# Kernel tuning notes

Measured on AMD Instinct MI355X. Metric: run time of the kernel, lower is better.

## Reference

```python
import jax, jax.numpy as jnp
import numpy as np

B, N, D, H, DH = 1, 192, 128, 4, 32
INNER = H * DH  # == D


def _ln(x, g, b):
    mu = x.mean(-1, keepdims=True)
    var = ((x - mu) ** 2).mean(-1, keepdims=True)
    return (x - mu) * jax.lax.rsqrt(var + 1e-5) * g + b


def _axial(x, row, lng, lnb, wq, wkv, wo, bo, wg, bg, wb):
    # x: (B, N, N, D). row=True: attend along axis 2 (rows as batch);
    # row=False: attend along axis 1 (columns as batch).
    scale = DH ** -0.5
    # edge bias from RAW x (edges are not layer-normed in the torch code)
    bias = jnp.einsum('bijd,dh->bhij', x, wb)            # (B, H, N, N)
    xn = _ln(x, lng, lnb)
    xa = xn if row else jnp.swapaxes(xn, 1, 2)           # (B, R, S, D)
    q = (xa @ wq).reshape(B, N, N, H, DH) * scale
    kv = (xa @ wkv).reshape(B, N, N, 2, H, DH)           # chunk(2): k then v
    k, v = kv[..., 0, :, :], kv[..., 1, :, :]
    # scores: (B, R, H, q, k); same bias matrix broadcast over every row/col R
    dots = jnp.einsum('brqhe,brkhe->brhqk', q, k) + bias[:, None]
    attn = jax.nn.softmax(dots, axis=-1)
    o = jnp.einsum('brhqk,brkhe->brqhe', attn, v).reshape(B, N, N, INNER)
    gates = jax.nn.sigmoid(xa @ wg + bg)                 # sigmoid gating on pre-attn x
    out = (o * gates) @ wo + bo
    return out if row else jnp.swapaxes(out, 1, 2)


def setup_inputs() -> dict:
    key = jax.random.key(0)
    ks = iter(jax.random.split(key, 32))

    def w(shape, s=0.02):
        return jax.random.normal(next(ks), shape, dtype=jnp.float32) * s

    inp = {"x": jax.random.normal(next(ks), (B, N, N, D), dtype=jnp.float32)}
    for sfx in ("o", "i"):  # outgoing (row) / ingoing (col) triangle attention
        inp[f"lng_{sfx}"] = jnp.ones((D,), jnp.float32)
        inp[f"lnb_{sfx}"] = jnp.zeros((D,), jnp.float32)
        inp[f"wq_{sfx}"] = w((D, INNER))
        inp[f"wkv_{sfx}"] = w((D, 2 * INNER))
        inp[f"wo_{sfx}"] = w((INNER, D))
        inp[f"bo_{sfx}"] = jnp.zeros((D,), jnp.float32)
        inp[f"wg_{sfx}"] = w((D, INNER))
        inp[f"bg_{sfx}"] = jnp.ones((INNER,), jnp.float32)  # gating bias init = 1
        inp[f"wb_{sfx}"] = w((D, H))
    inp["lng_f"] = jnp.ones((D,), jnp.float32)
    inp["lnb_f"] = jnp.zeros((D,), jnp.float32)
    inp["w1"] = w((D, 8 * D))      # dim -> dim*mult*2, mult=4
    inp["b1"] = jnp.zeros((8 * D,), jnp.float32)
    inp["w2"] = w((4 * D, D))
    inp["b2"] = jnp.zeros((D,), jnp.float32)
    return inp


def reference(x, lng_o, lnb_o, wq_o, wkv_o, wo_o, bo_o, wg_o, bg_o, wb_o,
              lng_i, lnb_i, wq_i, wkv_i, wo_i, bo_i, wg_i, bg_i, wb_i,
              lng_f, lnb_f, w1, b1, w2, b2):
    x = _axial(x, True, lng_o, lnb_o, wq_o, wkv_o, wo_o, bo_o, wg_o, bg_o, wb_o) + x
    x = _axial(x, False, lng_i, lnb_i, wq_i, wkv_i, wo_i, bo_i, wg_i, bg_i, wb_i) + x
    xn = _ln(x, lng_f, lnb_f)
    h = xn @ w1 + b1
    a, g = jnp.split(h, 2, axis=-1)   # GEGLU: x * gelu(gates), exact gelu
    ff = (a * jax.nn.gelu(g, approximate=False)) @ w2 + b2
    return x + ff
```

## Files before the change

kernel.cpp:

```cpp
#include <hip/hip_runtime.h>
#include <hip/hip_bf16.h>
#include <math.h>

constexpr int NSEQ = 192;
constexpr int DIM  = 128;
constexpr int NH   = 4;
constexpr int DHEAD = 32;
constexpr int MROWS = NSEQ * NSEQ;

typedef __hip_bfloat16 bf16;
typedef __attribute__((ext_vector_type(8))) short bf16x8;
typedef __attribute__((ext_vector_type(4))) float f32x4;
typedef unsigned int u32;

__device__ __forceinline__ void gload16(const void* g, void* l) {
    __builtin_amdgcn_global_load_lds(
        (const __attribute__((address_space(1))) u32*)g,
        (__attribute__((address_space(3))) u32*)l, 16, 0, 0);
}

__device__ __forceinline__ short f2bs(float f) {
    __hip_bfloat16 h = __float2bfloat16(f);
    return *(short*)&h;
}
__device__ __forceinline__ float bs2f(unsigned short s) {
    return __uint_as_float(((u32)s) << 16);
}

__global__ __launch_bounds__(256)
void prep_kernel(const float* __restrict__ wq_o, const float* __restrict__ wkv_o,
                 const float* __restrict__ wg_o,
                 const float* __restrict__ wq_i, const float* __restrict__ wkv_i,
                 const float* __restrict__ wg_i,
                 const float* __restrict__ wo_o, const float* __restrict__ wo_i,
                 const float* __restrict__ w1, const float* __restrict__ b1,
                 const float* __restrict__ w2,
                 bf16* __restrict__ WQKVG_O, bf16* __restrict__ WQKVG_I,
                 bf16* __restrict__ WOT_O, bf16* __restrict__ WOT_I,
                 bf16* __restrict__ W1PT, bf16* __restrict__ W2T,
                 float* __restrict__ B1P,
                 const float* __restrict__ x, const float* __restrict__ lng,
                 const float* __restrict__ lnb, const float* __restrict__ wb,
                 bf16* __restrict__ xa, bf16* __restrict__ bias,
                 bf16* __restrict__ xb)
{
    if (blockIdx.x < 1412) {
        int idx = blockIdx.x * 256 + threadIdx.x;
        const float scale = 0.17677669529663689f;
        if (idx < 131072) {
            int s = idx >> 16, i = idx & 65535;
            int r = i >> 7, d = i & 127;
            const float* wq  = s ? wq_i  : wq_o;
            const float* wkv = s ? wkv_i : wkv_o;
            const float* wg  = s ? wg_i  : wg_o;
            float v;
            if (r < 128)      v = wq[d * 128 + r] * scale;
            else if (r < 384) v = wkv[d * 256 + (r - 128)];
            else              v = wg[d * 128 + (r - 384)];
            (s ? WQKVG_I : WQKVG_O)[i] = __float2bfloat16(v);
        } else if (idx < 163840) {
            int i = idx - 131072; int s = i >> 14; i &= 16383;
            int r = i >> 7, d = i & 127;
            (s ? WOT_I : WOT_O)[i] = __float2bfloat16((s ? wo_i : wo_o)[d * 128 + r]);
        } else if (idx < 294912) {
            int i = idx - 163840;
            int r = i >> 7, d = i & 127;
            int col = (r & 1) ? 512 + (r >> 1) : (r >> 1);
            W1PT[i] = __float2bfloat16(w1[d * 1024 + col]);
        } else if (idx < 360448) {
            int i = idx - 294912;
            int n = i >> 9, k = i & 511;
            W2T[i] = __float2bfloat16(w2[k * 128 + n]);
        } else if (idx < 361472) {
            int r = idx - 360448;
            B1P[r] = b1[(r & 1) ? 512 + (r >> 1) : (r >> 1)];
        }
        return;
    }
    int wid  = threadIdx.x >> 6;
    int lane = threadIdx.x & 63;
    int row  = (blockIdx.x - 1412) * 4 + wid;
    const float* xr = x + (size_t)row * DIM;
    float2 xv = *(const float2*)(xr + lane * 2);
    float s = xv.x + xv.y, sq = xv.x * xv.x + xv.y * xv.y;
    #pragma unroll
    for (int off = 32; off > 0; off >>= 1) {
        s  += __shfl_down(s, off);
        sq += __shfl_down(sq, off);
    }
    s = __shfl(s, 0); sq = __shfl(sq, 0);
    float mu  = s * (1.0f / 128.0f);
    float var = sq * (1.0f / 128.0f) - mu * mu;
    float rs  = rsqrtf(var + 1e-5f);
    float2 gv = *(const float2*)(lng + lane * 2);
    float2 bv = *(const float2*)(lnb + lane * 2);
    float y0 = (xv.x - mu) * rs * gv.x + bv.x;
    float y1 = (xv.y - mu) * rs * gv.y + bv.y;
    u32 packed = (u32)(unsigned short)f2bs(y0) | ((u32)(unsigned short)f2bs(y1) << 16);
    *(u32*)(xa + (size_t)row * DIM + lane * 2) = packed;
    u32 packedx = (u32)(unsigned short)f2bs(xv.x) | ((u32)(unsigned short)f2bs(xv.y) << 16);
    *(u32*)(xb + (size_t)row * DIM + lane * 2) = packedx;
    float4 w0 = *(const float4*)(wb + lane * 8);
    float4 w1v = *(const float4*)(wb + lane * 8 + 4);
    #pragma unroll
    for (int h = 0; h < NH; ++h) {
        float bh = xv.x * ((const float*)&w0)[h] + xv.y * ((const float*)&w1v)[h];
        #pragma unroll
        for (int off = 32; off > 0; off >>= 1) bh += __shfl_down(bh, off);
        if (lane == 0) bias[(size_t)h * MROWS + row] = __float2bfloat16(bh);
    }
}

enum { EPI_QKVG = 0, EPI_OUT = 1, EPI_GEGLU = 2, EPI_FF2 = 3 };

template<int EPI, int BM, int K, int NSEG>
__global__ __launch_bounds__(256, 4)
void mfma_gemm(const bf16* __restrict__ A, const bf16* __restrict__ BT,
               const float* __restrict__ e_bias,
               const bf16* __restrict__ e_residb,
               float* __restrict__ e_outf,
               bf16* __restrict__ e_outb,
               bf16* __restrict__ e_outb2,
               const float* __restrict__ lng,
               const float* __restrict__ lnb,
               const float* __restrict__ wbp,
               bf16* __restrict__ biasb,
               bf16* __restrict__ xa,
               int trans)
{
    constexpr int MREP  = BM / 32;
    constexpr int AB    = BM * 128;
    constexpr int STAGE = AB + 16384;
    constexpr int EPIB  = (BM / 2) * 512;
    constexpr int LDSB  = STAGE > EPIB ? STAGE : EPIB;
    __shared__ char sm[LDSB];
    char* asb = sm;
    char* bsb = sm + AB;
    float* eb = (float*)sm;

    int tile, seg;
    if (NSEG == 1) { tile = blockIdx.x; seg = blockIdx.y; }
    else {
        constexpr int LS = (NSEG == 4) ? 2 : 3;
        int bid = blockIdx.x;
        seg  = (bid >> 3) & (NSEG - 1);
        tile = (bid & 7) + ((bid >> (3 + LS)) << 3);
    }
    int m0 = tile * BM, n0 = seg * 128;

    int tid = threadIdx.x;
    int l = tid & 63, w = tid >> 6;
    int wr = w >> 1, wc = w & 1;
    int fr = l & 15, g = l >> 4;
    int lr8 = l >> 3;
    int satom = (l & 7) ^ lr8;

    f32x4 acc[MREP][4] = {};

    for (int k0 = 0; k0 < K; k0 += 64) {
        #pragma unroll
        for (int i = 0; i < BM / 32; ++i)
            gload16(A + (size_t)(m0 + i * 32 + w * 8 + lr8) * K + k0 + satom * 8,
                    asb + i * 4096 + w * 1024);
        #pragma unroll
        for (int i = 0; i < 4; ++i)
            gload16(BT + (size_t)(n0 + i * 32 + w * 8 + lr8) * K + k0 + satom * 8,
                    bsb + i * 4096 + w * 1024);
        __syncthreads();
        #pragma unroll
        for (int kk = 0; kk < 2; ++kk) {
            bf16x8 af[MREP], bfr[4];
            #pragma unroll
            for (int mi = 0; mi < MREP; ++mi) {
                int r = wr * (BM / 2) + mi * 16 + fr;
                af[mi] = *(const bf16x8*)(asb + r * 128 + ((kk * 64 + g * 16) ^ ((r & 7) << 4)));
            }
            #pragma unroll
            for (int ni = 0; ni < 4; ++ni) {
                int r = wc * 64 + ni * 16 + fr;
                bfr[ni] = *(const bf16x8*)(bsb + r * 128 + ((kk * 64 + g * 16) ^ ((r & 7) << 4)));
            }
            #pragma unroll
            for (int mi = 0; mi < MREP; ++mi)
                #pragma unroll
                for (int ni = 0; ni < 4; ++ni)
                    acc[mi][ni] = __builtin_amdgcn_mfma_f32_16x16x32_bf16(
                        af[mi], bfr[ni], acc[mi][ni], 0, 0, 0);
        }
        __syncthreads();
    }

    #pragma unroll
    for (int rr = 0; rr < 2; ++rr) {
        if (wr == rr) {
            #pragma unroll
            for (int mi = 0; mi < MREP; ++mi)
                #pragma unroll
                for (int ni = 0; ni < 4; ++ni)
                    #pragma unroll
                    for (int j = 0; j < 4; ++j) {
                        int rl = mi * 16 + g * 4 + j;
                        int cl = wc * 64 + ni * 16 + fr;
                        int a  = cl >> 2;
                        int pa = (((a >> 2) + (a & 3)) & 7) | ((a & 3) << 3);
                        eb[rl * 128 + pa * 4 + (cl & 3)] = acc[mi][ni][j];
                    }
        }
        __syncthreads();
        #pragma unroll
        for (int p = 0; p < BM / 64; ++p) {
            int c = tid + p * 256;
            int row_l = c >> 3, ch = c & 7;
            int grow = m0 + rr * (BM / 2) + row_l;
            int gc0 = ch * 16;
            float v[16];
            #pragma unroll
            for (int q = 0; q < 4; ++q) {
                int pa = ((ch + q) & 7) + q * 8;
                f32x4 t4 = *(const f32x4*)&eb[row_l * 128 + pa * 4];
                v[q * 4 + 0] = t4[0]; v[q * 4 + 1] = t4[1];
                v[q * 4 + 2] = t4[2]; v[q * 4 + 3] = t4[3];
            }
            if (EPI == EPI_QKVG) {
                short o16[16];
                if (seg < 3) {
                    #pragma unroll
                    for (int i = 0; i < 16; ++i) o16[i] = f2bs(v[i]);
                    int h = ch >> 1, e0 = (ch & 1) * 16;
                    bf16* dst = e_outb + ((size_t)(seg * NH + h) * MROWS + grow) * DHEAD + e0;
                    *(uint4*)dst = *(uint4*)o16;
                    *(uint4*)(dst + 8) = *(uint4*)(o16 + 8);
                } else {
                    #pragma unroll
                    for (int i = 0; i < 16; ++i)
                        o16[i] = f2bs(1.0f / (1.0f + __expf(-(v[i] + e_bias[gc0 + i]))));
                    bf16* dst = e_outb2 + (size_t)grow * DIM + gc0;
                    *(uint4*)dst = *(uint4*)o16;
                    *(uint4*)(dst + 8) = *(uint4*)(o16 + 8);
                }
            } else if (EPI == EPI_OUT) {
                int orow  = trans ? ((grow % NSEQ) * NSEQ + grow / NSEQ) : grow;
                int xarow = (grow % NSEQ) * NSEQ + grow / NSEQ;
                unsigned short r16[16];
                const bf16* rp = e_residb + (size_t)orow * DIM + gc0;
                *(uint4*)r16 = *(const uint4*)rp;
                *(uint4*)(r16 + 8) = *(const uint4*)(rp + 8);
                short o16[16];
                #pragma unroll
                for (int i = 0; i < 16; ++i) {
                    v[i] += e_bias[gc0 + i] + bs2f(r16[i]);
                    o16[i] = f2bs(v[i]);
                }
                bf16* xo = e_outb + (size_t)orow * DIM + gc0;
                *(uint4*)xo = *(uint4*)o16;
                *(uint4*)(xo + 8) = *(uint4*)(o16 + 8);
                float s1 = 0.f, s2 = 0.f;
                #pragma unroll
                for (int i = 0; i < 16; ++i) { s1 += v[i]; s2 += v[i] * v[i]; }
                #pragma unroll
                for (int off = 1; off < 8; off <<= 1) {
                    s1 += __shfl_xor(s1, off);
                    s2 += __shfl_xor(s2, off);
                }
                float mu  = s1 * (1.0f / 128.0f);
                float var = s2 * (1.0f / 128.0f) - mu * mu;
                float rs  = rsqrtf(var + 1e-5f);
                #pragma unroll
                for (int i = 0; i < 16; ++i)
                    o16[i] = f2bs((v[i] - mu) * rs * lng[gc0 + i] + lnb[gc0 + i]);
                bf16* xd = xa + (size_t)xarow * DIM + gc0;
                *(uint4*)xd = *(uint4*)o16;
                *(uint4*)(xd + 8) = *(uint4*)(o16 + 8);
                if (wbp) {
                    float bh[NH] = {};
                    #pragma unroll
                    for (int i = 0; i < 16; ++i) {
                        float vv = v[i];
                        #pragma unroll
                        for (int h = 0; h < NH; ++h)
                            bh[h] = fmaf(vv, wbp[(gc0 + i) * NH + h], bh[h]);
                    }
                    #pragma unroll
                    for (int off = 1; off < 8; off <<= 1)
                        #pragma unroll
                        for (int h = 0; h < NH; ++h) bh[h] += __shfl_xor(bh[h], off);
                    if (ch == 0)
                        #pragma unroll
                        for (int h = 0; h < NH; ++h)
                            biasb[(size_t)h * MROWS + grow] = __float2bfloat16(bh[h]);
                }
            } else if (EPI == EPI_FF2) {
                unsigned short r16[16];
                const bf16* rp = e_residb + (size_t)grow * DIM + gc0;
                *(uint4*)r16 = *(const uint4*)rp;
                *(uint4*)(r16 + 8) = *(const uint4*)(rp + 8);
                float* op = e_outf + (size_t)grow * DIM + gc0;
                #pragma unroll
                for (int q = 0; q < 4; ++q) {
                    float4 o4;
                    o4.x = v[q*4+0] + e_bias[gc0 + q*4 + 0] + bs2f(r16[q*4+0]);
                    o4.y = v[q*4+1] + e_bias[gc0 + q*4 + 1] + bs2f(r16[q*4+1]);
                    o4.z = v[q*4+2] + e_bias[gc0 + q*4 + 2] + bs2f(r16[q*4+2]);
                    o4.w = v[q*4+3] + e_bias[gc0 + q*4 + 3] + bs2f(r16[q*4+3]);
                    *(float4*)(op + q * 4) = o4;
                }
            } else {
                short o8[8];
                #pragma unroll
                for (int t = 0; t < 8; ++t) {
                    float a  = v[2*t]     + e_bias[n0 + gc0 + 2*t];
                    float gg = v[2*t + 1] + e_bias[n0 + gc0 + 2*t + 1];
                    float y  = 1.5957691216f * (gg + 0.044715f * gg * gg * gg);
                    float ge = gg / (1.0f + __expf(-y));
                    o8[t] = f2bs(a * ge);
                }
                *(uint4*)(e_outb + (size_t)grow * 512 + ((n0 + gc0) >> 1)) = *(uint4*)o8;
            }
        }
        __syncthreads();
    }
}

__global__ __launch_bounds__(256)
void attn_mfma_kernel(const bf16* __restrict__ Qh, const bf16* __restrict__ Kh,
                      const bf16* __restrict__ Vh, const bf16* __restrict__ BIAS,
                      const bf16* __restrict__ G, bf16* __restrict__ TMP)
{
    __shared__ unsigned short vtp[32][200];
    int h = blockIdx.x / NSEQ;
    int r = blockIdx.x % NSEQ;
    int t = threadIdx.x;
    int l = t & 63;
    int w = t >> 6;

    const bf16* vbase = Vh + ((size_t)h * MROWS + (size_t)r * NSEQ) * DHEAD;
    #pragma unroll
    for (int i = 0; i < 6; ++i) {
        int q4 = t + i * 256;
        int k = q4 >> 3, e0 = (q4 & 7) * 4;
        uint2 v = *(const uint2*)(vbase + (size_t)k * DHEAD + e0);
        int kk = k & 31, sup = k >> 5;
        int col = sup * 32 + ((kk & 15) >> 2) * 8 + (kk & 3) + ((kk >> 4) << 2);
        const unsigned short* vs = (const unsigned short*)&v;
        #pragma unroll
        for (int j = 0; j < 4; ++j) vtp[e0 + j][col] = vs[j];
    }
    __syncthreads();

    int fr = l & 15, g = l >> 4;
    int q0 = w * 48;
    const bf16*  qbase = Qh + ((size_t)h * MROWS + (size_t)r * NSEQ) * DHEAD;
    const bf16*  kbase = Kh + ((size_t)h * MROWS + (size_t)r * NSEQ) * DHEAD;
    const bf16*  bbase = BIAS + (size_t)h * MROWS;

    bf16x8 qf[3];
    #pragma unroll
    for (int i = 0; i < 3; ++i)
        qf[i] = *(const bf16x8*)(qbase + (size_t)(q0 + i * 16 + fr) * DHEAD + g * 8);

    f32x4 ot[3][2] = {};
    float m_[3] = {-1e30f, -1e30f, -1e30f};
    float s_[3] = {};

    for (int sup = 0; sup < 6; ++sup) {
        bf16x8 kf0 = *(const bf16x8*)(kbase + (size_t)(sup * 32 + fr) * DHEAD + g * 8);
        bf16x8 kf1 = *(const bf16x8*)(kbase + (size_t)(sup * 32 + 16 + fr) * DHEAD + g * 8);
        bf16x8 pb[3];
        #pragma unroll
        for (int qt = 0; qt < 3; ++qt) {
            f32x4 z = {};
            f32x4 s0 = __builtin_amdgcn_mfma_f32_16x16x32_bf16(kf0, qf[qt], z, 0, 0, 0);
            f32x4 s1 = __builtin_amdgcn_mfma_f32_16x16x32_bf16(kf1, qf[qt], z, 0, 0, 0);
            const bf16* bp = bbase + (size_t)(q0 + qt * 16 + fr) * NSEQ + sup * 32 + g * 4;
            uint2 bb0 = *(const uint2*)bp;
            uint2 bb1 = *(const uint2*)(bp + 16);
            const unsigned short* b0s = (const unsigned short*)&bb0;
            const unsigned short* b1s = (const unsigned short*)&bb1;
            #pragma unroll
            for (int j = 0; j < 4; ++j) s0[j] += bs2f(b0s[j]);
            #pragma unroll
            for (int j = 0; j < 4; ++j) s1[j] += bs2f(b1s[j]);
            float tmax = fmaxf(fmaxf(fmaxf(s0[0], s0[1]), fmaxf(s0[2], s0[3])),
                               fmaxf(fmaxf(s1[0], s1[1]), fmaxf(s1[2], s1[3])));
            tmax = fmaxf(tmax, __shfl_xor(tmax, 16));
            tmax = fmaxf(tmax, __shfl_xor(tmax, 32));
            if (__any(tmax > m_[qt] + 8.0f)) {
                float mn = fmaxf(m_[qt], tmax);
                float c = __expf(m_[qt] - mn);
                s_[qt] *= c; ot[qt][0] *= c; ot[qt][1] *= c;
                m_[qt] = mn;
            }
            float p[8];
            #pragma unroll
            for (int j = 0; j < 4; ++j) p[j]     = __expf(s0[j] - m_[qt]);
            #pragma unroll
            for (int j = 0; j < 4; ++j) p[4 + j] = __expf(s1[j] - m_[qt]);
            s_[qt] += ((p[0] + p[1]) + (p[2] + p[3])) + ((p[4] + p[5]) + (p[6] + p[7]));
            bf16x8 pk;
            #pragma unroll
            for (int j = 0; j < 8; ++j) pk[j] = f2bs(p[j]);
            pb[qt] = pk;
        }
        #pragma unroll
        for (int et = 0; et < 2; ++et) {
            bf16x8 vf = *(const bf16x8*)(&vtp[et * 16 + fr][sup * 32 + g * 8]);
            #pragma unroll
            for (int qt = 0; qt < 3; ++qt)
                ot[qt][et] = __builtin_amdgcn_mfma_f32_16x16x32_bf16(vf, pb[qt], ot[qt][et], 0, 0, 0);
        }
    }

    #pragma unroll
    for (int qt = 0; qt < 3; ++qt) {
        float sq = s_[qt];
        sq += __shfl_xor(sq, 16);
        sq += __shfl_xor(sq, 32);
        float inv = 1.0f / sq;
        int q = q0 + qt * 16 + fr;
        size_t row = (size_t)r * NSEQ + q;
        #pragma unroll
        for (int et = 0; et < 2; ++et) {
            int e0 = h * DHEAD + et * 16 + g * 4;
            const bf16* gp = G + row * DIM + e0;
            u32 g01 = *(const u32*)gp;
            u32 g23 = *(const u32*)(gp + 2);
            float gx0 = __uint_as_float((g01 & 0xffffu) << 16);
            float gx1 = __uint_as_float(g01 & 0xffff0000u);
            float gx2 = __uint_as_float((g23 & 0xffffu) << 16);
            float gx3 = __uint_as_float(g23 & 0xffff0000u);
            short o4[4];
            o4[0] = f2bs(ot[qt][et][0] * inv * gx0);
            o4[1] = f2bs(ot[qt][et][1] * inv * gx1);
            o4[2] = f2bs(ot[qt][et][2] * inv * gx2);
            o4[3] = f2bs(ot[qt][et][3] * inv * gx3);
            *(uint2*)(TMP + row * DIM + e0) = *(uint2*)o4;
        }
    }
}

extern "C" void kernel_launch(void* const* d_in, const int* in_sizes, int n_in,
                              void* d_out, int out_size, void* d_ws, size_t ws_size,
                              hipStream_t stream) {
    const float* x     = (const float*)d_in[0];
    const float* lng_o = (const float*)d_in[1];
    const float* lnb_o = (const float*)d_in[2];
    const float* wq_o  = (const float*)d_in[3];
    const float* wkv_o = (const float*)d_in[4];
    const float* wo_o  = (const float*)d_in[5];
    const float* bo_o  = (const float*)d_in[6];
    const float* wg_o  = (const float*)d_in[7];
    const float* bg_o  = (const float*)d_in[8];
    const float* wb_o  = (const float*)d_in[9];
    const float* lng_i = (const float*)d_in[10];
    const float* lnb_i = (const float*)d_in[11];
    const float* wq_i  = (const float*)d_in[12];
    const float* wkv_i = (const float*)d_in[13];
    const float* wo_i  = (const float*)d_in[14];
    const float* bo_i  = (const float*)d_in[15];
    const float* wg_i  = (const float*)d_in[16];
    const float* bg_i  = (const float*)d_in[17];
    const float* wb_i  = (const float*)d_in[18];
    const float* lng_f = (const float*)d_in[19];
    const float* lnb_f = (const float*)d_in[20];
    const float* w1    = (const float*)d_in[21];
    const float* b1    = (const float*)d_in[22];
    const float* w2    = (const float*)d_in[23];
    const float* b2    = (const float*)d_in[24];

    const size_t T = (size_t)MROWS * DIM;
    char* base = (char*)d_ws;
    bf16*  XA    = (bf16*)base;  base += T * 2;
    bf16*  XB    = (bf16*)base;  base += T * 2;
    bf16*  X     = (bf16*)base;  base += T * 2;
    bf16*  QKVb  = (bf16*)base;  base += 3 * T * 2;
    bf16*  Gb    = (bf16*)base;  base += T * 2;
    bf16*  BIASb = (bf16*)base;  base += (size_t)NH * MROWS * 2;
    bf16*  TMP   = (bf16*)base;  base += T * 2;
    bf16*  WQKVG_O = (bf16*)base; base += 512 * 128 * 2;
    bf16*  WQKVG_I = (bf16*)base; base += 512 * 128 * 2;
    bf16*  WOT_O   = (bf16*)base; base += 128 * 128 * 2;
    bf16*  WOT_I   = (bf16*)base; base += 128 * 128 * 2;
    bf16*  W1PT    = (bf16*)base; base += 1024 * 128 * 2;
    bf16*  W2T     = (bf16*)base; base += 128 * 512 * 2;
    float* B1P     = (float*)base; base += 1024 * 4;
    bf16*  H2      = (bf16*)QKVb;
    bf16*  Qhp = QKVb;
    bf16*  Khp = QKVb + T;
    bf16*  Vhp = QKVb + 2 * T;

    prep_kernel<<<1412 + MROWS / 4, 256, 0, stream>>>(
        wq_o, wkv_o, wg_o, wq_i, wkv_i, wg_i, wo_o, wo_i, w1, b1, w2,
        WQKVG_O, WQKVG_I, WOT_O, WOT_I, W1PT, W2T, B1P,
        x, lng_o, lnb_o, wb_o, XA, BIASb, XB);

    dim3 gOUT(MROWS / 64, 1), gFF2(MROWS / 64, 1);

    mfma_gemm<EPI_QKVG, 128, 128, 4><<<(MROWS / 128) * 4, 256, 0, stream>>>(
        XA, WQKVG_O, bg_o, nullptr, nullptr, QKVb, Gb,
        nullptr, nullptr, nullptr, nullptr, nullptr, 0);
    attn_mfma_kernel<<<NSEQ * NH, 256, 0, stream>>>(Qhp, Khp, Vhp, BIASb, Gb, TMP);
    mfma_gemm<EPI_OUT, 64, 128, 1><<<gOUT, 256, 0, stream>>>(
        TMP, WOT_O, bo_o, XB, nullptr, X, nullptr,
        lng_i, lnb_i, wb_i, BIASb, XA, 0);

    mfma_gemm<EPI_QKVG, 128, 128, 4><<<(MROWS / 128) * 4, 256, 0, stream>>>(
        XA, WQKVG_I, bg_i, nullptr, nullptr, QKVb, Gb,
        nullptr, nullptr, nullptr, nullptr, nullptr, 0);
    attn_mfma_kernel<<<NSEQ * NH, 256, 0, stream>>>(Qhp, Khp, Vhp, BIASb, Gb, TMP);
    mfma_gemm<EPI_OUT, 64, 128, 1><<<gOUT, 256, 0, stream>>>(
        TMP, WOT_I, bo_i, X, nullptr, X, nullptr,
        lng_f, lnb_f, nullptr, nullptr, XA, 1);

    mfma_gemm<EPI_GEGLU, 128, 128, 8><<<(MROWS / 128) * 8, 256, 0, stream>>>(
        XA, W1PT, B1P, nullptr, nullptr, H2, nullptr,
        nullptr, nullptr, nullptr, nullptr, nullptr, 0);
    mfma_gemm<EPI_FF2, 64, 512, 1><<<gFF2, 256, 0, stream>>>(
        H2, W2T, b2, X, (float*)d_out, nullptr, nullptr,
        nullptr, nullptr, nullptr, nullptr, nullptr, 0);
}
```

Baseline: 193.3 us.

## Prefetch next K-tile into registers while computing current tile in GEMM

Replaces the per-iteration direct global-to-LDS loads with a register-staged software pipeline. The first K tile goes through global_load_lds, and later tiles are loaded into registers before the MFMA work on the current tile, then written to LDS after a barrier. This is meant to hide global memory latency behind compute. In exchange it uses more registers (AI+4 uint4 per thread), which may hurt occupancy under launch_bounds(256,4), and it adds a second barrier per step.

Result: slower. 255.9 us (+32.4%).

```diff
diff --git a/kernel.cpp b/kernel.cpp
--- a/kernel.cpp
+++ b/kernel.cpp
@@ -129,6 +129,8 @@
                int trans)
 {
     constexpr int MREP  = BM / 32;
+    constexpr int AI    = BM / 32;
+    constexpr int NSTEP = K / 64;
     constexpr int AB    = BM * 128;
     constexpr int STAGE = AB + 16384;
     constexpr int EPIB  = (BM / 2) * 512;
@@ -157,16 +159,28 @@
 
     f32x4 acc[MREP][4] = {};
 
-    for (int k0 = 0; k0 < K; k0 += 64) {
-        #pragma unroll
-        for (int i = 0; i < BM / 32; ++i)
-            gload16(A + (size_t)(m0 + i * 32 + w * 8 + lr8) * K + k0 + satom * 8,
-                    asb + i * 4096 + w * 1024);
-        #pragma unroll
-        for (int i = 0; i < 4; ++i)
-            gload16(BT + (size_t)(n0 + i * 32 + w * 8 + lr8) * K + k0 + satom * 8,
-                    bsb + i * 4096 + w * 1024);
-        __syncthreads();
+    #pragma unroll
+    for (int i = 0; i < AI; ++i)
+        gload16(A + (size_t)(m0 + i * 32 + w * 8 + lr8) * K + satom * 8,
+                asb + i * 4096 + w * 1024);
+    #pragma unroll
+    for (int i = 0; i < 4; ++i)
+        gload16(BT + (size_t)(n0 + i * 32 + w * 8 + lr8) * K + satom * 8,
+                bsb + i * 4096 + w * 1024);
+    __syncthreads();
+
+    uint4 ra[AI], rb[4];
+    #pragma unroll
+    for (int s = 0; s < NSTEP; ++s) {
+        if (s + 1 < NSTEP) {
+            int k1 = (s + 1) * 64;
+            #pragma unroll
+            for (int i = 0; i < AI; ++i)
+                ra[i] = *(const uint4*)(A + (size_t)(m0 + i * 32 + w * 8 + lr8) * K + k1 + satom * 8);
+            #pragma unroll
+            for (int i = 0; i < 4; ++i)
+                rb[i] = *(const uint4*)(BT + (size_t)(n0 + i * 32 + w * 8 + lr8) * K + k1 + satom * 8);
+        }
         #pragma unroll
         for (int kk = 0; kk < 2; ++kk) {
             bf16x8 af[MREP], bfr[4];
@@ -188,6 +202,15 @@
                         af[mi], bfr[ni], acc[mi][ni], 0, 0, 0);
         }
         __syncthreads();
+        if (s + 1 < NSTEP) {
+            #pragma unroll
+            for (int i = 0; i < AI; ++i)
+                *(uint4*)(asb + i * 4096 + w * 1024 + l * 16) = ra[i];
+            #pragma unroll
+            for (int i = 0; i < 4; ++i)
+                *(uint4*)(bsb + i * 4096 + w * 1024 + l * 16) = rb[i];
+            __syncthreads();
+        }
     }
 
     #pragma unroll
```
